# Performance work log

Measured on AMD Instinct MI355X. Metric: run time of the kernel, lower is better.

## Reference

```python
import jax, jax.numpy as jnp
import numpy as np

E = 8            # num experts
CAP_FACTOR = 1.5
K_THRESH = 0.8
BAL_ALPHA = 0.005
REG_ALPHA = 1e-6
BN_EPS = 1e-5
POOL = 16


def setup_inputs() -> dict:
    key = jax.random.key(0)
    ks = jax.random.split(key, 8)
    B, H, L, D = 128, 1024, 512, 1024
    return {
        "x": jax.random.normal(ks[0], (B, H, L), jnp.float32),
        "conv_w": jax.random.normal(ks[1], (64, H, 3), jnp.float32) / np.float32(np.sqrt(3 * H)),
        "conv_b": jnp.zeros((64,), jnp.float32),
        "bn_gamma": jnp.ones((64 * POOL,), jnp.float32),
        "bn_beta": jnp.zeros((64 * POOL,), jnp.float32),
        "fc1_w": jax.random.normal(ks[2], (128, 64 * POOL), jnp.float32) / np.float32(np.sqrt(64 * POOL)),
        "fc1_b": jnp.zeros((128,), jnp.float32),
        "fc2_w": jax.random.normal(ks[3], (E, 128), jnp.float32) / np.float32(np.sqrt(128)),
        "fc2_b": jnp.zeros((E,), jnp.float32),
        "exp_w": jax.random.normal(ks[4], (E, H, D), jnp.float32) / np.float32(np.sqrt(H)),
        "exp_b": jnp.zeros((E, D), jnp.float32),
    }


def _forward(x, conv_w, conv_b, bn_gamma, bn_beta, fc1_w, fc1_b, fc2_w, fc2_b, exp_w, exp_b):
    B, H, L = x.shape
    # ---- router: Conv1d(H->64,k=3,p=1) -> GELU -> AdaptiveAvgPool1d(16) -> Flatten -> BN -> FC -> GELU -> FC -> softmax
    h = jax.lax.conv_general_dilated(x, conv_w, (1,), ((1, 1),),
                                     dimension_numbers=("NCH", "OIH", "NCH"))
    h = jax.nn.gelu(h + conv_b[None, :, None], approximate=False)          # [B,64,L]; torch GELU is exact erf
    h = h.reshape(B, 64, POOL, L // POOL).mean(-1).reshape(B, 64 * POOL)   # adaptive avg pool (L%16==0) + flatten
    mu, var = h.mean(0), h.var(0)                                          # training-mode (Sync)BatchNorm: batch stats
    h = (h - mu) / jnp.sqrt(var + BN_EPS) * bn_gamma + bn_beta
    h = jax.nn.gelu(h @ fc1_w.T + fc1_b, approximate=False)
    rw = jax.nn.softmax(h @ fc2_w.T + fc2_b, axis=1)                       # [B,E]; expert dropout = identity (eval)
    # ---- dynamic k: smallest k s.t. cumsum of sorted probs > threshold; only max over batch is used
    topk_w, topk_idx = jax.lax.top_k(rw, E)                                # full descending sort
    cum = jnp.cumsum(topk_w, axis=1)
    over = cum > K_THRESH
    k_per = jnp.where(jnp.any(over, axis=1), jnp.argmax(over, axis=1) + 1, E)
    max_k = jnp.max(jnp.clip(k_per, 1, E))
    col_valid = jnp.arange(E)[None, :] < max_k                             # broadcast [B,E]; cols >= max_k unused
    assign = jnp.where(col_valid, topk_idx, -1)
    # ---- capacity enforcement: per expert keep the `capacity` highest-weight assignments, drop the rest (-1)
    capacity = max(1, int(B * CAP_FACTOR / E))
    flat_idx, flat_w = assign.reshape(-1), topk_w.reshape(-1)              # row-major [B*E], matches torch flatten

    def keep_for_expert(e):
        m = flat_idx == e
        order = jnp.argsort(-jnp.where(m, flat_w, -jnp.inf))               # descending within expert e
        ranks = jnp.zeros_like(order).at[order].set(jnp.arange(order.shape[0]))
        return m & (ranks < capacity)

    keep = jax.vmap(keep_for_expert)(jnp.arange(E))                        # [E, B*E]
    counts = keep.sum(axis=1).astype(jnp.float32)                          # == bincount of valid final indices
    final_idx = jnp.where(jnp.any(keep, axis=0), flat_idx, -1).reshape(B, E)
    # ---- experts: mean-pool over length, per-expert Linear(H->D); gather each sample's selected experts
    pooled = x.mean(axis=2)                                                # [B,H]
    y = jnp.einsum("bh,ehd->bed", pooled, exp_w) + exp_b[None]             # [B,E,D] all-expert outputs
    outputs = jnp.take_along_axis(y, jnp.clip(final_idx, 0)[..., None], axis=1)
    outputs = jnp.where(final_idx[..., None] >= 0, outputs, 0.0)           # dropped slots contribute zeros
    # ---- combine: softmax over the max_k slots; dropped (-1) slots enter softmax with logit 0, as in torch
    logits = jnp.where(col_valid, topk_w * (final_idx >= 0), -jnp.inf)
    norm_w = jax.nn.softmax(logits, axis=1)                                # [B,E]
    pooler = jnp.einsum("bkd,bk->bd", outputs, norm_w)                     # [B,D]
    # ---- losses / stats
    usage = rw.mean(0)
    reg = jnp.sum(exp_w * exp_w) + jnp.sum(exp_b * exp_b)                  # sum ||param||_2^2 over expert params
    added_loss = BAL_ALPHA * jnp.var(usage, ddof=1) + REG_ALPHA * reg      # torch.var is unbiased
    return pooler, added_loss, usage, counts


def reference(x, conv_w, conv_b, bn_gamma, bn_beta, fc1_w, fc1_b, fc2_w, fc2_b, exp_w, exp_b):
    return _forward(x, conv_w, conv_b, bn_gamma, bn_beta, fc1_w, fc1_b, fc2_w, fc2_b, exp_w, exp_b)
```

## Files before the change

kernel.cpp:

```cpp
#include <hip/hip_runtime.h>
#include <hip/hip_bf16.h>
#include <math.h>

#define NB 128
#define NH 1024
#define NL 512
#define OC 64
#define NE 8
#define ND 1024
#define CAPACITY 24

static const size_t WS_PART  = 0;
static const size_t WS_WSEP  = 1048576;
static const size_t WS_PXT   = 2097152;
static const size_t WS_HPOOL = 2228224;
static const size_t WS_SCALE = 2359296;
static const size_t WS_SHIFT = 2360320;
static const size_t WS_A1    = 2361344;
static const size_t WS_USAGE = 2379784;
static const size_t WS_VARU  = 2379792;
static const size_t WS_REG   = 2379793;
static const size_t WS_CNT   = 2379794;
static const size_t WS_WMAT  = 2380832;

typedef __attribute__((ext_vector_type(8))) short bf16x8;
typedef __attribute__((ext_vector_type(4))) float f32x4;

__device__ __forceinline__ float gelu_exact(float v) {
    return 0.5f * v * (1.0f + erff(v * 0.70710678118654752440f));
}

__device__ __forceinline__ unsigned short f2bf_rne(float f) {
    unsigned int u = __float_as_uint(f);
    unsigned int r = u + 0x7FFFu + ((u >> 16) & 1u);
    return (unsigned short)(r >> 16);
}
__device__ __forceinline__ float bf2f(unsigned short h) {
    return __uint_as_float(((unsigned int)h) << 16);
}

__device__ __forceinline__ unsigned cvtpk_bf16(float a, float b) {
    unsigned r;
    asm("v_cvt_pk_bf16_f32 %0, %1, %2" : "=v"(r) : "v"(a), "v"(b));
    return r;
}

__global__ __launch_bounds__(256) void k_wsplit(const float* __restrict__ cw, float* __restrict__ ws)
{
    if (blockIdx.x == 0 && threadIdx.x == 0) ws[WS_REG] = 0.0f;
    unsigned short* wsep = (unsigned short*)(ws + WS_WSEP);
    int i = blockIdx.x * 256 + threadIdx.x;
    float v = cw[i];
    int j = i % 3;
    int t = i / 3;
    int h = t & 1023;
    int o = t >> 10;
    int it = h >> 5;
    int h5 = h & 31;
    int e = h5 & 7;
    int lane = (o & 15) | ((h5 >> 3) << 4);
    int mt = (o >> 4) & 3;
    unsigned short hi = f2bf_rne(v);
    unsigned short lo = f2bf_rne(v - bf2f(hi));
    size_t base = ((size_t)((it * 3 + j) * 4 + mt) * 2) * 512 + lane * 8 + e;
    wsep[base] = hi;
    wsep[base + 512] = lo;
}

__device__ __forceinline__ void cvt_unit(unsigned int* X, int lq, int h4,
                                         const float4* v, float* sh)
{
    sh[0] = sh[1] = sh[2] = sh[3] = 0.f;
#pragma unroll
    for (int i = 0; i < 4; ++i) {
        float a0 = ((const float*)&v[0])[i];
        float a1 = ((const float*)&v[1])[i];
        float a2 = ((const float*)&v[2])[i];
        float a3 = ((const float*)&v[3])[i];
        sh[0] += a0; sh[1] += a1; sh[2] += a2; sh[3] += a3;
        unsigned h01 = cvtpk_bf16(a0, a1);
        unsigned h23 = cvtpk_bf16(a2, a3);
        float r0 = a0 - __uint_as_float(h01 << 16);
        float r1 = a1 - __uint_as_float(h01 & 0xFFFF0000u);
        float r2 = a2 - __uint_as_float(h23 << 16);
        float r3 = a3 - __uint_as_float(h23 & 0xFFFF0000u);
        unsigned l01 = cvtpk_bf16(r0, r1);
        unsigned l23 = cvtpk_bf16(r2, r3);
        int r = lq * 4 + i;
        unsigned int* dst = X + r * 34 + ((2 * h4) ^ ((r & 3) << 2));
        *(uint2*)dst = make_uint2(h01, h23);
        *(uint2*)(dst + 16) = make_uint2(l01, l23);
    }
}

__global__ __launch_bounds__(256, 2) void k_convmfma(const float* __restrict__ x,
                                                     const float* __restrict__ cb,
                                                     float* __restrict__ ws)
{
    __shared__ unsigned int Xb[2][136 * 34];
    __shared__ float xs2[3][128];
    __shared__ float scb[64];

    const int lc = blockIdx.x, b = blockIdx.y;
    const int l0 = lc * 128;
    const int tid = threadIdx.x;
    const int wv = tid >> 6, lane = tid & 63;
    const int h4 = tid & 7;
    const int lqi = 1 + (tid >> 3);
    const bool has_halo = (tid < 16);
    const int lqh = (tid < 8) ? 0 : 33;
    const bool halo_ok = (tid < 8) ? (lc > 0) : (lc < 3);

    const unsigned short* wsg = (const unsigned short*)(ws + WS_WSEP);
    const float* xbase = x + (size_t)b * (NH * NL);
    float* poolp = ws + WS_PART + ((size_t)(lc * 128 + b)) * 1024;

    if (tid < 64) scb[tid] = cb[tid];

    f32x4 acc[4][2];
#pragma unroll
    for (int mt = 0; mt < 4; ++mt)
#pragma unroll
        for (int nt = 0; nt < 2; ++nt) acc[mt][nt] = (f32x4){0.f, 0.f, 0.f, 0.f};

    float4 xA[4], hA[4], xB[4], hB[4];

    auto xload = [&](int itL, float4* xc, float4* hc) {
        const int hn = itL * 32;
        const float* p = xbase + (size_t)(hn + h4 * 4) * NL + (l0 - 4 + lqi * 4);
#pragma unroll
        for (int jj = 0; jj < 4; ++jj) xc[jj] = *(const float4*)(p + jj * NL);
        if (has_halo) {
            int gl = l0 - 4 + lqh * 4;
#pragma unroll
            for (int jj = 0; jj < 4; ++jj)
                hc[jj] = halo_ok ? *(const float4*)(xbase + (size_t)(hn + h4 * 4 + jj) * NL + gl)
                                 : make_float4(0.f, 0.f, 0.f, 0.f);
        }
    };

    auto body = [&](int it, float4* xc, float4* hc) {
        unsigned int* Xw = Xb[it & 1];
        bf16x8 Ar[3][4][2];
        {
            const unsigned short* abase = wsg + (size_t)it * 12288 + lane * 8;
#pragma unroll
            for (int j = 0; j < 3; ++j)
#pragma unroll
                for (int mt = 0; mt < 4; ++mt) {
                    Ar[j][mt][0] = *(const bf16x8*)(abase + (size_t)(j * 8 + mt * 2) * 512);
                    Ar[j][mt][1] = *(const bf16x8*)(abase + (size_t)(j * 8 + mt * 2 + 1) * 512);
                }
        }
        {
            float sh[4];
            cvt_unit(Xw, lqi, h4, xc, sh);
#pragma unroll
            for (int jj = 0; jj < 4; ++jj) {
                float s = sh[jj];
                s += __shfl_xor(s, 8, 64);
                s += __shfl_xor(s, 16, 64);
                s += __shfl_xor(s, 32, 64);
                if ((lane >> 3) == 0) xs2[it % 3][wv * 32 + h4 * 4 + jj] = s;
            }
            if (has_halo) { float d[4]; cvt_unit(Xw, lqh, h4, hc, d); }
        }
        __syncthreads();
        if (it > 0 && tid < 32) {
            const float* S = xs2[(it - 1) % 3];
            poolp[(it - 1) * 32 + tid] = S[tid] + S[32 + tid] + S[64 + tid] + S[96 + tid];
        }
        if (it < 30) xload(it + 2, xc, hc);
        const int g4 = (lane >> 4) << 2;
#pragma unroll
        for (int j = 0; j < 3; ++j) {
            bf16x8 Bh[2], Bl[2];
#pragma unroll
            for (int nt = 0; nt < 2; ++nt) {
                int rx = 3 + j + wv * 32 + nt * 16 + (lane & 15);
                const unsigned int* bp = Xw + rx * 34 + (g4 ^ ((rx & 3) << 2));
                Bh[nt] = *(const bf16x8*)bp;
                Bl[nt] = *(const bf16x8*)(bp + 16);
            }
#pragma unroll
            for (int mt = 0; mt < 4; ++mt)
#pragma unroll
                for (int nt = 0; nt < 2; ++nt) {
                    acc[mt][nt] = __builtin_amdgcn_mfma_f32_16x16x32_bf16(Ar[j][mt][0], Bh[nt], acc[mt][nt], 0, 0, 0);
                    acc[mt][nt] = __builtin_amdgcn_mfma_f32_16x16x32_bf16(Ar[j][mt][0], Bl[nt], acc[mt][nt], 0, 0, 0);
                    acc[mt][nt] = __builtin_amdgcn_mfma_f32_16x16x32_bf16(Ar[j][mt][1], Bh[nt], acc[mt][nt], 0, 0, 0);
                }
        }
    };

    xload(0, xA, hA);
    xload(1, xB, hB);

    for (int it2 = 0; it2 < 32; it2 += 2) {
        body(it2, xA, hA);
        body(it2 + 1, xB, hB);
    }
    if (tid < 32) {
        const float* S = xs2[31 % 3];
        poolp[31 * 32 + tid] = S[tid] + S[32 + tid] + S[64 + tid] + S[96 + tid];
    }

    {
        const int g = lane >> 4, cidx = lane & 15;
#pragma unroll
        for (int mt = 0; mt < 4; ++mt) {
            float s[4];
#pragma unroll
            for (int r = 0; r < 4; ++r) {
                int o = mt * 16 + g * 4 + r;
                float bo = scb[o];
                s[r] = gelu_exact(acc[mt][0][r] + bo) + gelu_exact(acc[mt][1][r] + bo);
            }
#pragma unroll
            for (int m = 1; m < 16; m <<= 1) {
#pragma unroll
                for (int r = 0; r < 4; ++r) s[r] += __shfl_xor(s[r], m, 64);
            }
            if (cidx == 0) {
#pragma unroll
                for (int r = 0; r < 4; ++r) {
                    int o = mt * 16 + g * 4 + r;
                    ws[WS_HPOOL + (size_t)b * 1024 + o * 16 + lc * 4 + wv] = s[r] * (1.0f / 32.0f);
                }
            }
        }
    }
}

__global__ __launch_bounds__(256) void k_mid(const float* __restrict__ g,
                                             const float* __restrict__ bet,
                                             float* __restrict__ ws)
{
    int bx = blockIdx.x;
    if (bx < 512) {
        int id = bx * 256 + threadIdx.x;
        int b = id >> 10, h = id & 1023;
        float s = 0.0f;
#pragma unroll
        for (int lcc = 0; lcc < 4; lcc++) s += ws[WS_PART + ((size_t)(lcc * 128 + b)) * 1024 + h];
        ws[WS_PXT + (size_t)h * 128 + b] = s * (1.0f / 512.0f);
    } else {
        int f = (bx - 512) * 256 + threadIdx.x;
        const float* hp = ws + WS_HPOOL;
        float s = 0.0f;
        for (int b = 0; b < 128; b++) s += hp[(size_t)b * 1024 + f];
        float mu = s * (1.0f / 128.0f);
        float v = 0.0f;
        for (int b = 0; b < 128; b++) { float d = hp[(size_t)b * 1024 + f] - mu; v += d * d; }
        float var = v * (1.0f / 128.0f);
        float sc = g[f] / sqrtf(var + 1e-5f);
        ws[WS_SCALE + f] = sc;
        ws[WS_SHIFT + f] = bet[f] - mu * sc;
    }
}

__global__ __launch_bounds__(256) void k_fc1(const float* __restrict__ w1,
                                             const float* __restrict__ b1,
                                             float* __restrict__ ws)
{
    __shared__ float hb[1024];
    __shared__ float red[256];
    int b = blockIdx.x, tid = threadIdx.x;
    const float* hp = ws + WS_HPOOL + (size_t)b * 1024;
    for (int k = tid; k < 1024; k += 256)
        hb[k] = hp[k] * ws[WS_SCALE + k] + ws[WS_SHIFT + k];
    __syncthreads();
    int o = tid & 127, kh = tid >> 7;
    const float4* wrp = (const float4*)(w1 + (size_t)o * 1024 + kh * 512);
    const float* hx = hb + kh * 512;
    float acc = 0.0f;
#pragma unroll 4
    for (int k = 0; k < 128; k++) {
        float4 w = wrp[k];
        acc = fmaf(hx[4 * k], w.x, acc);     acc = fmaf(hx[4 * k + 1], w.y, acc);
        acc = fmaf(hx[4 * k + 2], w.z, acc); acc = fmaf(hx[4 * k + 3], w.w, acc);
    }
    red[tid] = acc;
    __syncthreads();
    if (tid < 128) {
        float v = red[tid] + red[tid + 128] + b1[tid];
        ws[WS_A1 + (size_t)b * 128 + tid] = gelu_exact(v);
    }
}

__global__ __launch_bounds__(128) void k_route(const float* __restrict__ w2,
                                               const float* __restrict__ b2,
                                               float* __restrict__ ws)
{
    __shared__ float w2s[1024];
    __shared__ float red[1024];
    __shared__ float tkw_s[1024];
    __shared__ int   tki_s[1024];
    __shared__ int   keep_s[1024];
    __shared__ float wv_s[128];
    __shared__ int   sv_s[128];
    __shared__ float usg[8];
    __shared__ int   cnt_s[8];
    __shared__ int   mk;

    const int tid = threadIdx.x;
    const int b = tid;
    for (int i = tid; i < 1024; i += 128) w2s[i] = w2[i];
    if (tid == 0) mk = 0;
    if (tid < 8) cnt_s[tid] = 0;
    __syncthreads();

    const float* ar = ws + WS_A1 + (size_t)b * 128;
    float rw[8];
    float m = -1e30f;
#pragma unroll
    for (int e = 0; e < 8; e++) {
        float acc = b2[e];
        for (int k = 0; k < 128; k++) acc = fmaf(ar[k], w2s[e * 128 + k], acc);
        rw[e] = acc;
        m = fmaxf(m, acc);
    }
    float s = 0.0f;
#pragma unroll
    for (int e = 0; e < 8; e++) { rw[e] = expf(rw[e] - m); s += rw[e]; }
    float inv = 1.0f / s;
#pragma unroll
    for (int e = 0; e < 8; e++) rw[e] *= inv;
#pragma unroll
    for (int e = 0; e < 8; e++) red[e * 128 + b] = rw[e];

    float tw[8]; int ti[8]; unsigned used = 0;
#pragma unroll
    for (int r = 0; r < 8; r++) {
        float bv = -1e30f; int bi = 0;
#pragma unroll
        for (int e = 0; e < 8; e++) {
            bool take = !((used >> e) & 1u) && (rw[e] > bv);
            bv = take ? rw[e] : bv;
            bi = take ? e : bi;
        }
        used |= (1u << bi);
        tw[r] = bv; ti[r] = bi;
    }
    float cum = 0.0f; int kp = 8;
#pragma unroll
    for (int r = 0; r < 8; r++) {
        cum += tw[r];
        if (cum > 0.8f) { kp = r + 1; break; }
    }
    atomicMax(&mk, kp);
#pragma unroll
    for (int r = 0; r < 8; r++) { tkw_s[b * 8 + r] = tw[r]; tki_s[b * 8 + r] = ti[r]; }
    __syncthreads();

    if (tid < 8) {
        float s2 = 0.0f;
        for (int bb = 0; bb < 128; bb++) s2 += red[tid * 128 + bb];
        float u = s2 * (1.0f / 128.0f);
        usg[tid] = u;
        ws[WS_USAGE + tid] = u;
    }
    __syncthreads();
    if (tid == 0) {
        float mu = 0.0f;
#pragma unroll
        for (int e = 0; e < 8; e++) mu += usg[e];
        mu *= (1.0f / 8.0f);
        float v = 0.0f;
#pragma unroll
        for (int e = 0; e < 8; e++) { float d = usg[e] - mu; v += d * d; }
        ws[WS_VARU] = v * (1.0f / 7.0f);
    }

    const int maxk = mk;
    for (int e = 0; e < 8; ++e) {
        float myw = 0.0f; int mys = -1;
        for (int k = 0; k < maxk; k++)
            if (tki_s[b * 8 + k] == e) { myw = tkw_s[b * 8 + k]; mys = b * 8 + k; }
        wv_s[b] = myw; sv_s[b] = mys;
        __syncthreads();
        if (mys >= 0) {
            int rank = 0;
            for (int b2 = 0; b2 < 128; b2++) {
                int s2 = sv_s[b2];
                if (s2 >= 0) {
                    float w2v = wv_s[b2];
                    if (w2v > myw || (w2v == myw && s2 < mys)) rank++;
                }
            }
            int kept = (rank < CAPACITY) ? 1 : 0;
            keep_s[mys] = kept;
            if (kept) atomicAdd(&cnt_s[e], 1);
        }
        __syncthreads();
    }
    if (tid < 8) ws[WS_CNT + tid] = (float)cnt_s[tid];

    float lv[8]; int kept[8]; int idx[8];
#pragma unroll
    for (int k = 0; k < 8; k++) {
        if (k < maxk) {
            kept[k] = keep_s[b * 8 + k];
            idx[k] = tki_s[b * 8 + k];
            lv[k] = kept[k] ? tkw_s[b * 8 + k] : 0.0f;
        } else { kept[k] = 0; idx[k] = -1; lv[k] = -1e30f; }
    }
    float mx = -1e30f;
#pragma unroll
    for (int k = 0; k < 8; k++) if (k < maxk) mx = fmaxf(mx, lv[k]);
    float s3 = 0.0f; float ev[8];
#pragma unroll
    for (int k = 0; k < 8; k++) { ev[k] = (k < maxk) ? expf(lv[k] - mx) : 0.0f; s3 += ev[k]; }
    float inv3 = 1.0f / s3;
    float Wr[8] = {0, 0, 0, 0, 0, 0, 0, 0};
#pragma unroll
    for (int k = 0; k < 8; k++) {
        if (kept[k]) {
            float v = ev[k] * inv3;
#pragma unroll
            for (int e = 0; e < 8; e++) Wr[e] += (idx[k] == e) ? v : 0.0f;
        }
    }
#pragma unroll
    for (int e = 0; e < 8; e++) ws[WS_WMAT + b * 8 + e] = Wr[e];
}

__global__ __launch_bounds__(256) void k_gemm(const float* __restrict__ ew,
                                              const float* __restrict__ eb,
                                              float* __restrict__ ws)
{
    __shared__ float a_s[32 * 128];
    __shared__ float b_s[32 * 32];
    __shared__ float w_s[1024];
    __shared__ float red2[256];
    const int blk = blockIdx.x;
    const int ks = blk >> 5, dt = blk & 31;
    const int tid = threadIdx.x;
    const int tb = tid >> 3, td = tid & 7;
    for (int i = tid; i < 1024; i += 256) w_s[i] = ws[WS_WMAT + i];
    float acc[4][4];
#pragma unroll
    for (int i = 0; i < 4; i++)
#pragma unroll
        for (int j = 0; j < 4; j++) acc[i][j] = 0.0f;
    float ssq = 0.0f;

    const float* pxt = ws + WS_PXT;
    for (int kt = 0; kt < 512; kt += 32) {
        __syncthreads();
        for (int idx = tid; idx < 4096; idx += 256) {
            int kk = idx >> 7, bb = idx & 127;
            int k = ks * 512 + kt + kk;
            int e = k >> 10, h = k & 1023;
            a_s[kk * 128 + bb] = w_s[bb * 8 + e] * pxt[(size_t)h * 128 + bb];
        }
        for (int idx = tid; idx < 1024; idx += 256) {
            int kk = idx >> 5, d = idx & 31;
            float v = ew[(size_t)(ks * 512 + kt + kk) * 1024 + dt * 32 + d];
            b_s[kk * 32 + d] = v;
            ssq += v * v;
        }
        __syncthreads();
#pragma unroll 4
        for (int kk = 0; kk < 32; kk++) {
            float4 av = *(const float4*)&a_s[kk * 128 + tb * 4];
            float4 bv = *(const float4*)&b_s[kk * 32 + td * 4];
            float aa[4] = {av.x, av.y, av.z, av.w};
            float bb4[4] = {bv.x, bv.y, bv.z, bv.w};
#pragma unroll
            for (int i = 0; i < 4; i++)
#pragma unroll
                for (int j = 0; j < 4; j++) acc[i][j] = fmaf(aa[i], bb4[j], acc[i][j]);
        }
    }
    float* outp = ws + WS_PART + (size_t)blk * 4096;
#pragma unroll
    for (int i = 0; i < 4; i++) {
        int bb = tb * 4 + i;
        *(float4*)(outp + bb * 32 + td * 4) = make_float4(acc[i][0], acc[i][1], acc[i][2], acc[i][3]);
    }
    if (blk == 0)
        for (int i = tid; i < 8192; i += 256) { float v = eb[i]; ssq += v * v; }
    red2[tid] = ssq;
    __syncthreads();
    for (int off = 128; off > 0; off >>= 1) {
        if (tid < off) red2[tid] += red2[tid + off];
        __syncthreads();
    }
    if (tid == 0) atomicAdd(ws + WS_REG, red2[0]);
}

__global__ __launch_bounds__(256) void k_final(const float* __restrict__ eb,
                                               const float* __restrict__ ws,
                                               float* __restrict__ out)
{
    int id = blockIdx.x * 256 + threadIdx.x;
    int b = id >> 10, d = id & 1023;
    int dt = d >> 5, dd = d & 31;
    float s = 0.0f;
#pragma unroll
    for (int ks = 0; ks < 16; ks++)
        s += ws[WS_PART + ((size_t)(ks * 32 + dt)) * 4096 + b * 32 + dd];
    float bias = 0.0f;
#pragma unroll
    for (int e = 0; e < 8; e++)
        bias += ws[WS_WMAT + b * 8 + e] * eb[(size_t)e * 1024 + d];
    out[id] = s + bias;
    if (blockIdx.x == 0) {
        int t = threadIdx.x;
        if (t == 0) out[131072] = 0.005f * ws[WS_VARU] + 1e-6f * ws[WS_REG];
        else if (t >= 1 && t < 9)  out[131072 + t] = ws[WS_USAGE + t - 1];
        else if (t >= 9 && t < 17) out[131072 + t] = ws[WS_CNT + t - 9];
    }
}

extern "C" void kernel_launch(void* const* d_in, const int* in_sizes, int n_in,
                              void* d_out, int out_size, void* d_ws, size_t ws_size,
                              hipStream_t stream)
{
    const float* x   = (const float*)d_in[0];
    const float* cw  = (const float*)d_in[1];
    const float* cb  = (const float*)d_in[2];
    const float* bng = (const float*)d_in[3];
    const float* bnb = (const float*)d_in[4];
    const float* f1w = (const float*)d_in[5];
    const float* f1b = (const float*)d_in[6];
    const float* f2w = (const float*)d_in[7];
    const float* f2b = (const float*)d_in[8];
    const float* ew  = (const float*)d_in[9];
    const float* eb  = (const float*)d_in[10];
    float* ws  = (float*)d_ws;
    float* out = (float*)d_out;

    k_wsplit  <<<768, 256, 0, stream>>>(cw, ws);
    k_convmfma<<<dim3(4, 128), 256, 0, stream>>>(x, cb, ws);
    k_mid     <<<516, 256, 0, stream>>>(bng, bnb, ws);
    k_fc1     <<<128, 256, 0, stream>>>(f1w, f1b, ws);
    k_route   <<<1, 128, 0, stream>>>(f2w, f2b, ws);
    k_gemm    <<<512, 256, 0, stream>>>(ew, eb, ws);
    k_final   <<<512, 256, 0, stream>>>(eb, ws, out);
}
```

Before: 321.6 us.

## Stream conv input via global_load_lds DMA and software-pipeline weight fragments

```diff
diff --git a/kernel.cpp b/kernel.cpp
--- a/kernel.cpp
+++ b/kernel.cpp
@@ -43,6 +43,13 @@
     unsigned r;
     asm("v_cvt_pk_bf16_f32 %0, %1, %2" : "=v"(r) : "v"(a), "v"(b));
     return r;
+}
+
+__device__ __forceinline__ void gload_lds16(const void* gsrc, void* ldst) {
+    __builtin_amdgcn_global_load_lds(
+        (const __attribute__((address_space(1))) void*)gsrc,
+        (__attribute__((address_space(3))) void*)ldst,
+        16, 0, 0);
 }
 
 __global__ __launch_bounds__(256) void k_wsplit(const float* __restrict__ cw, float* __restrict__ ws)
@@ -97,19 +104,17 @@
                                                      const float* __restrict__ cb,
                                                      float* __restrict__ ws)
 {
+    __shared__ float F[2][4352];
     __shared__ unsigned int Xb[2][136 * 34];
-    __shared__ float xs2[3][128];
+    __shared__ float xs2[3][32];
     __shared__ float scb[64];
 
     const int lc = blockIdx.x, b = blockIdx.y;
     const int l0 = lc * 128;
     const int tid = threadIdx.x;
     const int wv = tid >> 6, lane = tid & 63;
-    const int h4 = tid & 7;
-    const int lqi = 1 + (tid >> 3);
-    const bool has_halo = (tid < 16);
-    const int lqh = (tid < 8) ? 0 : 33;
-    const bool halo_ok = (tid < 8) ? (lc > 0) : (lc < 3);
+    const int hg = tid >> 5;
+    const int lq = (tid & 31) + 1;
 
     const unsigned short* wsg = (const unsigned short*)(ws + WS_WSEP);
     const float* xbase = x + (size_t)b * (NH * NL);
@@ -123,87 +128,118 @@
 #pragma unroll
         for (int nt = 0; nt < 2; ++nt) acc[mt][nt] = (f32x4){0.f, 0.f, 0.f, 0.f};
 
-    float4 xA[4], hA[4], xB[4], hB[4];
-
-    auto xload = [&](int itL, float4* xc, float4* hc) {
-        const int hn = itL * 32;
-        const float* p = xbase + (size_t)(hn + h4 * 4) * NL + (l0 - 4 + lqi * 4);
-#pragma unroll
-        for (int jj = 0; jj < 4; ++jj) xc[jj] = *(const float4*)(p + jj * NL);
-        if (has_halo) {
-            int gl = l0 - 4 + lqh * 4;
-#pragma unroll
-            for (int jj = 0; jj < 4; ++jj)
-                hc[jj] = halo_ok ? *(const float4*)(xbase + (size_t)(hn + h4 * 4 + jj) * NL + gl)
-                                 : make_float4(0.f, 0.f, 0.f, 0.f);
+    bf16x8 S0[4], S1[4];
+    bf16x8 Bh[2], Bl[2];
+    const int g4 = (lane >> 4) << 2;
+
+    auto xdma = [&](int itL) {
+        float* dstB = F[itL & 1];
+        const int ht = itL * 32;
+#pragma unroll
+        for (int c = 0; c < 5; ++c) {
+            int call = c * 4 + wv;
+            if (call < 17) {
+                int idx = call * 64 + lane;
+                int h = idx / 34;
+                int q = idx - h * 34;
+                int lpos = l0 - 4 + q * 4;
+                int lcl = min(max(lpos, 0), NL - 4);
+                gload_lds16(xbase + (size_t)(ht + h) * NL + lcl, dstB + call * 256);
+            }
         }
     };
 
-    auto body = [&](int it, float4* xc, float4* hc) {
-        unsigned int* Xw = Xb[it & 1];
-        bf16x8 Ar[3][4][2];
-        {
-            const unsigned short* abase = wsg + (size_t)it * 12288 + lane * 8;
-#pragma unroll
-            for (int j = 0; j < 3; ++j)
-#pragma unroll
-                for (int mt = 0; mt < 4; ++mt) {
-                    Ar[j][mt][0] = *(const bf16x8*)(abase + (size_t)(j * 8 + mt * 2) * 512);
-                    Ar[j][mt][1] = *(const bf16x8*)(abase + (size_t)(j * 8 + mt * 2 + 1) * 512);
-                }
-        }
-        {
-            float sh[4];
-            cvt_unit(Xw, lqi, h4, xc, sh);
-#pragma unroll
-            for (int jj = 0; jj < 4; ++jj) {
-                float s = sh[jj];
-                s += __shfl_xor(s, 8, 64);
-                s += __shfl_xor(s, 16, 64);
-                s += __shfl_xor(s, 32, 64);
-                if ((lane >> 3) == 0) xs2[it % 3][wv * 32 + h4 * 4 + jj] = s;
+    auto loadU = [&](int itL, int u, bf16x8* S) {
+        const unsigned short* p = wsg + (size_t)itL * 12288 + u * 2048 + lane * 8;
+        S[0] = *(const bf16x8*)(p);
+        S[1] = *(const bf16x8*)(p + 512);
+        S[2] = *(const bf16x8*)(p + 1024);
+        S[3] = *(const bf16x8*)(p + 1536);
+    };
+
+    auto loadB = [&](int j, int itL) {
+        const unsigned int* Xr = Xb[itL & 1];
+#pragma unroll
+        for (int nt = 0; nt < 2; ++nt) {
+            int rx = 3 + j + wv * 32 + nt * 16 + (lane & 15);
+            const unsigned int* bp = Xr + rx * 34 + (g4 ^ ((rx & 3) << 2));
+            Bh[nt] = *(const bf16x8*)bp;
+            Bl[nt] = *(const bf16x8*)(bp + 16);
+        }
+    };
+
+    auto mfmaU = [&](int hp, const bf16x8* S) {
+#pragma unroll
+        for (int m = 0; m < 2; ++m) {
+            const int mt = hp * 2 + m;
+#pragma unroll
+            for (int nt = 0; nt < 2; ++nt) {
+                acc[mt][nt] = __builtin_amdgcn_mfma_f32_16x16x32_bf16(S[2 * m],     Bh[nt], acc[mt][nt], 0, 0, 0);
+                acc[mt][nt] = __builtin_amdgcn_mfma_f32_16x16x32_bf16(S[2 * m],     Bl[nt], acc[mt][nt], 0, 0, 0);
+                acc[mt][nt] = __builtin_amdgcn_mfma_f32_16x16x32_bf16(S[2 * m + 1], Bh[nt], acc[mt][nt], 0, 0, 0);
             }
-            if (has_halo) { float d[4]; cvt_unit(Xw, lqh, h4, hc, d); }
-        }
+        }
+    };
+
+    auto cvt = [&](int itL) {
+        const float* Fs = F[itL & 1];
+        unsigned int* Xw = Xb[itL & 1];
+        float4 v[4];
+#pragma unroll
+        for (int r = 0; r < 4; ++r)
+            v[r] = *(const float4*)(Fs + ((hg * 4 + r) * 34 + lq) * 4);
+        float sh[4];
+        cvt_unit(Xw, lq, hg, v, sh);
+#pragma unroll
+        for (int r = 0; r < 4; ++r) {
+            float s = sh[r];
+            s += __shfl_xor(s, 1, 64);
+            s += __shfl_xor(s, 2, 64);
+            s += __shfl_xor(s, 4, 64);
+            s += __shfl_xor(s, 8, 64);
+            s += __shfl_xor(s, 16, 64);
+            if ((lane & 31) == 0)
+                xs2[itL % 3][(wv * 2 + (lane >> 5)) * 4 + r] = s;
+        }
+        if (tid < 16) {
+            int hgh = tid & 7;
+            int lqh = (tid < 8) ? 0 : 33;
+            bool ok = (tid < 8) ? (lc > 0) : (lc < 3);
+            float4 hv[4];
+#pragma unroll
+            for (int r = 0; r < 4; ++r)
+                hv[r] = ok ? *(const float4*)(Fs + ((hgh * 4 + r) * 34 + lqh) * 4)
+                           : make_float4(0.f, 0.f, 0.f, 0.f);
+            float d[4];
+            cvt_unit(Xw, lqh, hgh, hv, d);
+        }
+    };
+
+    xdma(0);
+    xdma(1);
+    loadU(0, 0, S0);
+    __syncthreads();
+
+    for (int it = 0; it < 32; ++it) {
+        cvt(it);
         __syncthreads();
-        if (it > 0 && tid < 32) {
-            const float* S = xs2[(it - 1) % 3];
-            poolp[(it - 1) * 32 + tid] = S[tid] + S[32 + tid] + S[64 + tid] + S[96 + tid];
-        }
-        if (it < 30) xload(it + 2, xc, hc);
-        const int g4 = (lane >> 4) << 2;
-#pragma unroll
-        for (int j = 0; j < 3; ++j) {
-            bf16x8 Bh[2], Bl[2];
-#pragma unroll
-            for (int nt = 0; nt < 2; ++nt) {
-                int rx = 3 + j + wv * 32 + nt * 16 + (lane & 15);
-                const unsigned int* bp = Xw + rx * 34 + (g4 ^ ((rx & 3) << 2));
-                Bh[nt] = *(const bf16x8*)bp;
-                Bl[nt] = *(const bf16x8*)(bp + 16);
-            }
-#pragma unroll
-            for (int mt = 0; mt < 4; ++mt)
-#pragma unroll
-                for (int nt = 0; nt < 2; ++nt) {
-                    acc[mt][nt] = __builtin_amdgcn_mfma_f32_16x16x32_bf16(Ar[j][mt][0], Bh[nt], acc[mt][nt], 0, 0, 0);
-                    acc[mt][nt] = __builtin_amdgcn_mfma_f32_16x16x32_bf16(Ar[j][mt][0], Bl[nt], acc[mt][nt], 0, 0, 0);
-                    acc[mt][nt] = __builtin_amdgcn_mfma_f32_16x16x32_bf16(Ar[j][mt][1], Bh[nt], acc[mt][nt], 0, 0, 0);
-                }
-        }
-    };
-
-    xload(0, xA, hA);
-    xload(1, xB, hB);
-
-    for (int it2 = 0; it2 < 32; it2 += 2) {
-        body(it2, xA, hA);
-        body(it2 + 1, xB, hB);
-    }
-    if (tid < 32) {
-        const float* S = xs2[31 % 3];
-        poolp[31 * 32 + tid] = S[tid] + S[32 + tid] + S[64 + tid] + S[96 + tid];
-    }
+        if (it > 0 && tid < 32)
+            poolp[(it - 1) * 32 + tid] = xs2[(it - 1) % 3][tid];
+
+        loadB(0, it);
+        loadU(it, 1, S1);  mfmaU(0, S0);
+        loadU(it, 2, S0);  mfmaU(1, S1);
+        loadB(1, it);
+        loadU(it, 3, S1);  mfmaU(0, S0);
+        loadU(it, 4, S0);  mfmaU(1, S1);
+        loadB(2, it);
+        loadU(it, 5, S1);  mfmaU(0, S0);
+        if (it < 30) xdma(it + 2);
+        if (it < 31) loadU(it + 1, 0, S0);
+        mfmaU(1, S1);
+    }
+    if (tid < 32)
+        poolp[31 * 32 + tid] = xs2[31 % 3][tid];
 
     {
         const int g = lane >> 4, cidx = lane & 15;
```

Result: slower. 344.7 us (+7.2%).

## Compute all-expert outputs independent of routing and overlap with router kernel

Applied to the files above, without the earlier changes.

```diff
diff --git a/kernel.cpp b/kernel.cpp
--- a/kernel.cpp
+++ b/kernel.cpp
@@ -17,11 +17,15 @@
 static const size_t WS_SCALE = 2359296;
 static const size_t WS_SHIFT = 2360320;
 static const size_t WS_A1    = 2361344;
+static const size_t WS_TKW   = 2377728;
+static const size_t WS_TKI   = 2378752;
 static const size_t WS_USAGE = 2379784;
 static const size_t WS_VARU  = 2379792;
 static const size_t WS_REG   = 2379793;
 static const size_t WS_CNT   = 2379794;
 static const size_t WS_WMAT  = 2380832;
+static const size_t WS_RW    = 2381856;
+static const size_t WS_KP    = 2382880;
 
 typedef __attribute__((ext_vector_type(8))) short bf16x8;
 typedef __attribute__((ext_vector_type(4))) float f32x4;
@@ -259,41 +263,151 @@
     }
 }
 
-__global__ __launch_bounds__(256) void k_fc1(const float* __restrict__ w1,
-                                             const float* __restrict__ b1,
-                                             float* __restrict__ ws)
-{
-    __shared__ float hb[1024];
-    __shared__ float red[256];
-    int b = blockIdx.x, tid = threadIdx.x;
-    const float* hp = ws + WS_HPOOL + (size_t)b * 1024;
-    for (int k = tid; k < 1024; k += 256)
-        hb[k] = hp[k] * ws[WS_SCALE + k] + ws[WS_SHIFT + k];
-    __syncthreads();
-    int o = tid & 127, kh = tid >> 7;
-    const float4* wrp = (const float4*)(w1 + (size_t)o * 1024 + kh * 512);
-    const float* hx = hb + kh * 512;
-    float acc = 0.0f;
+__global__ __launch_bounds__(256) void k_fused(const float* __restrict__ w1,
+                                               const float* __restrict__ b1,
+                                               const float* __restrict__ w2,
+                                               const float* __restrict__ b2,
+                                               const float* __restrict__ ew,
+                                               const float* __restrict__ eb,
+                                               float* __restrict__ ws)
+{
+    __shared__ float smem[6400];
+    const int bx = blockIdx.x;
+    const int tid = threadIdx.x;
+
+    if (bx < 256) {
+        float* a_s = smem;
+        float* b_s = smem + 4096;
+        float* red2 = smem + 6144;
+        const int e = bx >> 5, dt = (bx >> 1) & 15, ks = bx & 1;
+        const int tb = tid >> 3, td = tid & 7;
+        float acc[4][8];
+#pragma unroll
+        for (int i = 0; i < 4; i++)
+#pragma unroll
+            for (int j = 0; j < 8; j++) acc[i][j] = 0.0f;
+        float ssq = 0.0f;
+
+        const float* pxt = ws + WS_PXT;
+        for (int kt = 0; kt < 512; kt += 32) {
+            __syncthreads();
+            for (int idx = tid; idx < 4096; idx += 256) {
+                int kk = idx >> 7, bb = idx & 127;
+                a_s[kk * 128 + bb] = pxt[(size_t)(ks * 512 + kt + kk) * 128 + bb];
+            }
+            for (int idx = tid; idx < 2048; idx += 256) {
+                int kk = idx >> 6, d = idx & 63;
+                float v = ew[(size_t)e * 1048576 + (size_t)(ks * 512 + kt + kk) * 1024 + dt * 64 + d];
+                b_s[kk * 64 + d] = v;
+                ssq += v * v;
+            }
+            __syncthreads();
 #pragma unroll 4
-    for (int k = 0; k < 128; k++) {
-        float4 w = wrp[k];
-        acc = fmaf(hx[4 * k], w.x, acc);     acc = fmaf(hx[4 * k + 1], w.y, acc);
-        acc = fmaf(hx[4 * k + 2], w.z, acc); acc = fmaf(hx[4 * k + 3], w.w, acc);
-    }
-    red[tid] = acc;
-    __syncthreads();
-    if (tid < 128) {
-        float v = red[tid] + red[tid + 128] + b1[tid];
-        ws[WS_A1 + (size_t)b * 128 + tid] = gelu_exact(v);
-    }
-}
-
-__global__ __launch_bounds__(128) void k_route(const float* __restrict__ w2,
-                                               const float* __restrict__ b2,
-                                               float* __restrict__ ws)
-{
-    __shared__ float w2s[1024];
-    __shared__ float red[1024];
+            for (int kk = 0; kk < 32; kk++) {
+                float4 av = *(const float4*)&a_s[kk * 128 + tb * 4];
+                float4 b0 = *(const float4*)&b_s[kk * 64 + td * 8];
+                float4 b1v = *(const float4*)&b_s[kk * 64 + td * 8 + 4];
+                float aa[4] = {av.x, av.y, av.z, av.w};
+                float bb4[8] = {b0.x, b0.y, b0.z, b0.w, b1v.x, b1v.y, b1v.z, b1v.w};
+#pragma unroll
+                for (int i = 0; i < 4; i++)
+#pragma unroll
+                    for (int j = 0; j < 8; j++) acc[i][j] = fmaf(aa[i], bb4[j], acc[i][j]);
+            }
+        }
+        float* outp = ws + WS_PART + ((size_t)(ks * 8 + e) * 128) * 1024 + dt * 64;
+#pragma unroll
+        for (int i = 0; i < 4; i++) {
+            int bb = tb * 4 + i;
+            *(float4*)(outp + (size_t)bb * 1024 + td * 8) =
+                make_float4(acc[i][0], acc[i][1], acc[i][2], acc[i][3]);
+            *(float4*)(outp + (size_t)bb * 1024 + td * 8 + 4) =
+                make_float4(acc[i][4], acc[i][5], acc[i][6], acc[i][7]);
+        }
+        if (bx == 0)
+            for (int i = tid; i < 8192; i += 256) { float v = eb[i]; ssq += v * v; }
+        red2[tid] = ssq;
+        __syncthreads();
+        for (int off = 128; off > 0; off >>= 1) {
+            if (tid < off) red2[tid] += red2[tid + off];
+            __syncthreads();
+        }
+        if (tid == 0) atomicAdd(ws + WS_REG, red2[0]);
+    } else {
+        float* hb  = smem;
+        float* red = smem + 1024;
+        float* ha  = smem + 1280;
+        float* w2s = smem + 1408;
+        float* lg  = smem + 2432;
+        const int b = bx - 256;
+        const float* hp = ws + WS_HPOOL + (size_t)b * 1024;
+        for (int k = tid; k < 1024; k += 256)
+            hb[k] = hp[k] * ws[WS_SCALE + k] + ws[WS_SHIFT + k];
+        for (int i = tid; i < 1024; i += 256) w2s[i] = w2[i];
+        __syncthreads();
+        int o = tid & 127, kh = tid >> 7;
+        const float4* wrp = (const float4*)(w1 + (size_t)o * 1024 + kh * 512);
+        const float* hx = hb + kh * 512;
+        float acc = 0.0f;
+#pragma unroll 4
+        for (int k = 0; k < 128; k++) {
+            float4 w = wrp[k];
+            acc = fmaf(hx[4 * k], w.x, acc);     acc = fmaf(hx[4 * k + 1], w.y, acc);
+            acc = fmaf(hx[4 * k + 2], w.z, acc); acc = fmaf(hx[4 * k + 3], w.w, acc);
+        }
+        red[tid] = acc;
+        __syncthreads();
+        if (tid < 128)
+            ha[tid] = gelu_exact(red[tid] + red[tid + 128] + b1[tid]);
+        __syncthreads();
+        if (tid < 8) {
+            float a2 = b2[tid];
+            for (int k = 0; k < 128; k++) a2 = fmaf(ha[k], w2s[tid * 128 + k], a2);
+            lg[tid] = a2;
+        }
+        __syncthreads();
+        if (tid == 0) {
+            float rw[8];
+            float m = -1e30f;
+#pragma unroll
+            for (int e = 0; e < 8; e++) m = fmaxf(m, lg[e]);
+            float s = 0.0f;
+#pragma unroll
+            for (int e = 0; e < 8; e++) { rw[e] = expf(lg[e] - m); s += rw[e]; }
+            float inv = 1.0f / s;
+#pragma unroll
+            for (int e = 0; e < 8; e++) { rw[e] *= inv; ws[WS_RW + b * 8 + e] = rw[e]; }
+            float tw[8]; int ti[8]; unsigned used = 0;
+#pragma unroll
+            for (int r = 0; r < 8; r++) {
+                float bv = -1e30f; int bi = 0;
+#pragma unroll
+                for (int e = 0; e < 8; e++) {
+                    bool take = !((used >> e) & 1u) && (rw[e] > bv);
+                    bv = take ? rw[e] : bv;
+                    bi = take ? e : bi;
+                }
+                used |= (1u << bi);
+                tw[r] = bv; ti[r] = bi;
+            }
+            float cum = 0.0f; int kp = 8;
+#pragma unroll
+            for (int r = 0; r < 8; r++) {
+                cum += tw[r];
+                if (cum > 0.8f) { kp = r + 1; break; }
+            }
+#pragma unroll
+            for (int r = 0; r < 8; r++) {
+                ws[WS_TKW + b * 8 + r] = tw[r];
+                ((int*)ws)[WS_TKI + b * 8 + r] = ti[r];
+            }
+            ((int*)ws)[WS_KP + b] = kp;
+        }
+    }
+}
+
+__global__ __launch_bounds__(128) void k_route(float* __restrict__ ws)
+{
     __shared__ float tkw_s[1024];
     __shared__ int   tki_s[1024];
     __shared__ int   keep_s[1024];
@@ -305,57 +419,21 @@
 
     const int tid = threadIdx.x;
     const int b = tid;
-    for (int i = tid; i < 1024; i += 128) w2s[i] = w2[i];
     if (tid == 0) mk = 0;
     if (tid < 8) cnt_s[tid] = 0;
     __syncthreads();
-
-    const float* ar = ws + WS_A1 + (size_t)b * 128;
-    float rw[8];
-    float m = -1e30f;
-#pragma unroll
-    for (int e = 0; e < 8; e++) {
-        float acc = b2[e];
-        for (int k = 0; k < 128; k++) acc = fmaf(ar[k], w2s[e * 128 + k], acc);
-        rw[e] = acc;
-        m = fmaxf(m, acc);
-    }
-    float s = 0.0f;
-#pragma unroll
-    for (int e = 0; e < 8; e++) { rw[e] = expf(rw[e] - m); s += rw[e]; }
-    float inv = 1.0f / s;
-#pragma unroll
-    for (int e = 0; e < 8; e++) rw[e] *= inv;
-#pragma unroll
-    for (int e = 0; e < 8; e++) red[e * 128 + b] = rw[e];
-
-    float tw[8]; int ti[8]; unsigned used = 0;
+    atomicMax(&mk, ((const int*)ws)[WS_KP + b]);
 #pragma unroll
     for (int r = 0; r < 8; r++) {
-        float bv = -1e30f; int bi = 0;
-#pragma unroll
-        for (int e = 0; e < 8; e++) {
-            bool take = !((used >> e) & 1u) && (rw[e] > bv);
-            bv = take ? rw[e] : bv;
-            bi = take ? e : bi;
-        }
-        used |= (1u << bi);
-        tw[r] = bv; ti[r] = bi;
-    }
-    float cum = 0.0f; int kp = 8;
-#pragma unroll
-    for (int r = 0; r < 8; r++) {
-        cum += tw[r];
-        if (cum > 0.8f) { kp = r + 1; break; }
-    }
-    atomicMax(&mk, kp);
-#pragma unroll
-    for (int r = 0; r < 8; r++) { tkw_s[b * 8 + r] = tw[r]; tki_s[b * 8 + r] = ti[r]; }
+        tkw_s[b * 8 + r] = ws[WS_TKW + b * 8 + r];
+        tki_s[b * 8 + r] = ((const int*)ws)[WS_TKI + b * 8 + r];
+    }
     __syncthreads();
+    const int maxk = mk;
 
     if (tid < 8) {
         float s2 = 0.0f;
-        for (int bb = 0; bb < 128; bb++) s2 += red[tid * 128 + bb];
+        for (int bb = 0; bb < 128; bb++) s2 += ws[WS_RW + bb * 8 + tid];
         float u = s2 * (1.0f / 128.0f);
         usg[tid] = u;
         ws[WS_USAGE + tid] = u;
@@ -372,7 +450,6 @@
         ws[WS_VARU] = v * (1.0f / 7.0f);
     }
 
-    const int maxk = mk;
     for (int e = 0; e < 8; ++e) {
         float myw = 0.0f; int mys = -1;
         for (int k = 0; k < maxk; k++)
@@ -425,87 +502,23 @@
     for (int e = 0; e < 8; e++) ws[WS_WMAT + b * 8 + e] = Wr[e];
 }
 
-__global__ __launch_bounds__(256) void k_gemm(const float* __restrict__ ew,
-                                              const float* __restrict__ eb,
-                                              float* __restrict__ ws)
-{
-    __shared__ float a_s[32 * 128];
-    __shared__ float b_s[32 * 32];
-    __shared__ float w_s[1024];
-    __shared__ float red2[256];
-    const int blk = blockIdx.x;
-    const int ks = blk >> 5, dt = blk & 31;
-    const int tid = threadIdx.x;
-    const int tb = tid >> 3, td = tid & 7;
-    for (int i = tid; i < 1024; i += 256) w_s[i] = ws[WS_WMAT + i];
-    float acc[4][4];
-#pragma unroll
-    for (int i = 0; i < 4; i++)
-#pragma unroll
-        for (int j = 0; j < 4; j++) acc[i][j] = 0.0f;
-    float ssq = 0.0f;
-
-    const float* pxt = ws + WS_PXT;
-    for (int kt = 0; kt < 512; kt += 32) {
-        __syncthreads();
-        for (int idx = tid; idx < 4096; idx += 256) {
-            int kk = idx >> 7, bb = idx & 127;
-            int k = ks * 512 + kt + kk;
-            int e = k >> 10, h = k & 1023;
-            a_s[kk * 128 + bb] = w_s[bb * 8 + e] * pxt[(size_t)h * 128 + bb];
-        }
-        for (int idx = tid; idx < 1024; idx += 256) {
-            int kk = idx >> 5, d = idx & 31;
-            float v = ew[(size_t)(ks * 512 + kt + kk) * 1024 + dt * 32 + d];
-            b_s[kk * 32 + d] = v;
-            ssq += v * v;
-        }
-        __syncthreads();
-#pragma unroll 4
-        for (int kk = 0; kk < 32; kk++) {
-            float4 av = *(const float4*)&a_s[kk * 128 + tb * 4];
-            float4 bv = *(const float4*)&b_s[kk * 32 + td * 4];
-            float aa[4] = {av.x, av.y, av.z, av.w};
-            float bb4[4] = {bv.x, bv.y, bv.z, bv.w};
-#pragma unroll
-            for (int i = 0; i < 4; i++)
-#pragma unroll
-                for (int j = 0; j < 4; j++) acc[i][j] = fmaf(aa[i], bb4[j], acc[i][j]);
-        }
-    }
-    float* outp = ws + WS_PART + (size_t)blk * 4096;
-#pragma unroll
-    for (int i = 0; i < 4; i++) {
-        int bb = tb * 4 + i;
-        *(float4*)(outp + bb * 32 + td * 4) = make_float4(acc[i][0], acc[i][1], acc[i][2], acc[i][3]);
-    }
-    if (blk == 0)
-        for (int i = tid; i < 8192; i += 256) { float v = eb[i]; ssq += v * v; }
-    red2[tid] = ssq;
-    __syncthreads();
-    for (int off = 128; off > 0; off >>= 1) {
-        if (tid < off) red2[tid] += red2[tid + off];
-        __syncthreads();
-    }
-    if (tid == 0) atomicAdd(ws + WS_REG, red2[0]);
-}
-
 __global__ __launch_bounds__(256) void k_final(const float* __restrict__ eb,
                                                const float* __restrict__ ws,
                                                float* __restrict__ out)
 {
     int id = blockIdx.x * 256 + threadIdx.x;
     int b = id >> 10, d = id & 1023;
-    int dt = d >> 5, dd = d & 31;
+    const float* wm = ws + WS_WMAT + b * 8;
+    const float* Y = ws + WS_PART;
     float s = 0.0f;
 #pragma unroll
-    for (int ks = 0; ks < 16; ks++)
-        s += ws[WS_PART + ((size_t)(ks * 32 + dt)) * 4096 + b * 32 + dd];
-    float bias = 0.0f;
-#pragma unroll
-    for (int e = 0; e < 8; e++)
-        bias += ws[WS_WMAT + b * 8 + e] * eb[(size_t)e * 1024 + d];
-    out[id] = s + bias;
+    for (int e = 0; e < 8; e++) {
+        float y = Y[((size_t)e * 128 + b) * 1024 + d]
+                + Y[((size_t)(8 + e) * 128 + b) * 1024 + d]
+                + eb[(size_t)e * 1024 + d];
+        s += wm[e] * y;
+    }
+    out[id] = s;
     if (blockIdx.x == 0) {
         int t = threadIdx.x;
         if (t == 0) out[131072] = 0.005f * ws[WS_VARU] + 1e-6f * ws[WS_REG];
@@ -535,8 +548,7 @@
     k_wsplit  <<<768, 256, 0, stream>>>(cw, ws);
     k_convmfma<<<dim3(4, 128), 256, 0, stream>>>(x, cb, ws);
     k_mid     <<<516, 256, 0, stream>>>(bng, bnb, ws);
-    k_fc1     <<<128, 256, 0, stream>>>(f1w, f1b, ws);
-    k_route   <<<1, 128, 0, stream>>>(f2w, f2b, ws);
-    k_gemm    <<<512, 256, 0, stream>>>(ew, eb, ws);
+    k_fused   <<<384, 256, 0, stream>>>(f1w, f1b, f2w, f2b, ew, eb, ws);
+    k_route   <<<1, 128, 0, stream>>>(ws);
     k_final   <<<512, 256, 0, stream>>>(eb, ws, out);
 }
```

Result: no change. 316.0 us (-1.7%).
